# Optimization experiments

Hardware: AMD Instinct MI355X
Metric: run time of the kernel (lower is better)

Reference implementation:

```python
import jax, jax.numpy as jnp
import numpy as np

NODE_TYPES = ["drug", "protein", "side_effect", "pathway"]
N = {"drug": 20000, "protein": 50000, "side_effect": 10000, "pathway": 3000}
# (src_type, dst_type) for: treats, targets, in_pathway, causes, rev_treats, rev_targets, rev_in_pathway
RELS = [("drug", "side_effect"), ("drug", "protein"), ("protein", "pathway"),
        ("protein", "side_effect"), ("side_effect", "drug"), ("protein", "drug"),
        ("pathway", "protein")]
E = [500000, 400000, 150000, 400000, 500000, 400000, 150000]
D_IN, H, O = 128, 256, 256
EPS = 1e-5


def setup_inputs() -> dict:
    key = jax.random.key(0)
    ks = iter(jax.random.split(key, 64))
    inp = {}
    for t in NODE_TYPES:
        inp["x_" + t] = jax.random.normal(next(ks), (N[t], D_IN), jnp.float32)
    for i, (st, dt) in enumerate(RELS):
        inp[f"src_{i}"] = jax.random.randint(next(ks), (E[i],), 0, N[st], jnp.int32)
        inp[f"dst_{i}"] = jax.random.randint(next(ks), (E[i],), 0, N[dt], jnp.int32)
    sc1 = float(1.0 / np.sqrt(D_IN))
    sc2 = float(1.0 / np.sqrt(H))
    inp["W1l"] = jax.random.uniform(next(ks), (7, D_IN, H), jnp.float32, -sc1, sc1)
    inp["W1r"] = jax.random.uniform(next(ks), (7, D_IN, H), jnp.float32, -sc1, sc1)
    inp["b1"] = jax.random.uniform(next(ks), (7, H), jnp.float32, -sc1, sc1)
    inp["W2l"] = jax.random.uniform(next(ks), (7, H, O), jnp.float32, -sc2, sc2)
    inp["W2r"] = jax.random.uniform(next(ks), (7, H, O), jnp.float32, -sc2, sc2)
    inp["b2"] = jax.random.uniform(next(ks), (7, O), jnp.float32, -sc2, sc2)
    inp["g1"] = jnp.ones((H,), jnp.float32)
    inp["beta1"] = jnp.zeros((H,), jnp.float32)
    inp["g2"] = jnp.ones((O,), jnp.float32)
    inp["beta2"] = jnp.zeros((O,), jnp.float32)
    return inp


def _sage_layer(xs, srcs, dsts, Wl, Wr, b):
    # Hetero SAGEConv: per relation, mean-aggregate src features at dst,
    # project, add root transform; sum over relations per dst type.
    out = {t: None for t in NODE_TYPES}
    for i, (st, dt) in enumerate(RELS):
        msg = xs[st][srcs[i]]                                             # [E_i, d] gather
        s = jax.ops.segment_sum(msg, dsts[i], num_segments=N[dt])         # scatter-add
        cnt = jax.ops.segment_sum(jnp.ones((msg.shape[0], 1), msg.dtype),
                                  dsts[i], num_segments=N[dt])
        mean = s / jnp.maximum(cnt, 1.0)                                  # SAGE default aggr='mean'
        rel = mean @ Wl[i] + b[i] + xs[dt] @ Wr[i]                        # lin_l(agg) + lin_r(x_dst)
        out[dt] = rel if out[dt] is None else out[dt] + rel               # HeteroConv aggr='sum'
    return out


def _bn_relu(v, g, beta):
    # training-mode BatchNorm1d (biased variance) + ReLU
    mu = v.mean(0)
    var = v.var(0)
    return jax.nn.relu((v - mu) * jax.lax.rsqrt(var + EPS) * g + beta)


def reference(x_drug, x_protein, x_side_effect, x_pathway,
              W1l, W1r, b1, W2l, W2r, b2, g1, beta1, g2, beta2,
              src_0, dst_0, src_1, dst_1, src_2, dst_2, src_3, dst_3,
              src_4, dst_4, src_5, dst_5, src_6, dst_6):
    xs = {"drug": x_drug, "protein": x_protein,
          "side_effect": x_side_effect, "pathway": x_pathway}
    srcs = [src_0, src_1, src_2, src_3, src_4, src_5, src_6]
    dsts = [dst_0, dst_1, dst_2, dst_3, dst_4, dst_5, dst_6]
    h = _sage_layer(xs, srcs, dsts, W1l, W1r, b1)
    h = {t: _bn_relu(v, g1, beta1) for t, v in h.items()}
    h = _sage_layer(h, srcs, dsts, W2l, W2r, b2)
    h = {t: _bn_relu(v, g2, beta2) for t, v in h.items()}
    return (h["drug"], h["protein"], h["side_effect"], h["pathway"])
```

## Files before the change

kernel.cpp:

```cpp
#include <hip/hip_runtime.h>

#define EPS_BN 1e-5f

typedef short bf16x8 __attribute__((ext_vector_type(8)));
typedef float f32x4 __attribute__((ext_vector_type(4)));

__device__ __forceinline__ unsigned short f2b(float f)
{
    union { float f; unsigned int u; } c; c.f = f;
    unsigned int u = c.u + 0x7FFFu + ((c.u >> 16) & 1u);
    return (unsigned short)(u >> 16);
}
__device__ __forceinline__ float blo(unsigned int u)
{
    union { unsigned int u; float f; } c; c.u = u << 16; return c.f;
}
__device__ __forceinline__ float bhi(unsigned int u)
{
    union { unsigned int u; float f; } c; c.u = u & 0xFFFF0000u; return c.f;
}

__device__ __forceinline__ float dot2bf(float acc, unsigned int a, unsigned int sel)
{
    asm("v_dot2_f32_bf16 %0, %1, %2, %0" : "+v"(acc) : "v"(a), "v"(sel));
    return acc;
}

__device__ __forceinline__ void async_ld16(const unsigned short* g, unsigned short* l)
{
    __builtin_amdgcn_global_load_lds(
        (const __attribute__((address_space(1))) unsigned int*)g,
        (__attribute__((address_space(3))) unsigned int*)l, 16, 0, 0);
}

__device__ __forceinline__ int relof_e(int e) {
    return (e>=500000)+(e>=900000)+(e>=1050000)+(e>=1450000)+(e>=1950000)+(e>=2350000);
}
__device__ __forceinline__ int relof_n(int i) {
    return (i>=10000)+(i>=60000)+(i>=63000)+(i>=73000)+(i>=93000)+(i>=113000);
}
__device__ __forceinline__ int eoff_of(int r) {
    return r<1?0 : r<2?500000 : r<3?900000 : r<4?1050000 : r<5?1450000 : r<6?1950000 : 2350000;
}
__device__ __forceinline__ int coff_of(int r) {
    return r<1?0 : r<2?10000 : r<3?60000 : r<4?63000 : r<5?73000 : r<6?93000 : 113000;
}
__device__ __forceinline__ int typ_of(int row) { return (row>=20000)+(row>=70000)+(row>=80000); }
__device__ __forceinline__ float invR_of(int t){ return t<1?5e-5f : t<2?2e-5f : t<3?1e-4f : (1.0f/3000.0f); }

struct Graph { const int* src[7]; const int* dst[7]; };

__device__ __forceinline__ void relptrs(const Graph& g, int r, const int*& sp, const int*& dp)
{
    sp = g.src[0]; dp = g.dst[0];
    if (r==1){sp=g.src[1];dp=g.dst[1];}
    if (r==2){sp=g.src[2];dp=g.dst[2];}
    if (r==3){sp=g.src[3];dp=g.dst[3];}
    if (r==4){sp=g.src[4];dp=g.dst[4];}
    if (r==5){sp=g.src[5];dp=g.dst[5];}
    if (r==6){sp=g.src[6];dp=g.dst[6];}
}

__global__ void count_all(Graph g, int* __restrict__ icnt)
{
    for (int e = blockIdx.x * blockDim.x + threadIdx.x; e < 2500000; e += gridDim.x * blockDim.x) {
        int r = relof_e(e);
        const int *sp, *dp; relptrs(g, r, sp, dp);
        int le = e - eoff_of(r);
        atomicAdd(&icnt[coff_of(r) + dp[le]], 1);
    }
}

__global__ __launch_bounds__(1024)
void scan1(const int* __restrict__ icnt, int* __restrict__ scanbuf, int* __restrict__ bsums)
{
    __shared__ int lds[1024];
    int tid = threadIdx.x;
    int gid = blockIdx.x * 1024 + tid;
    int v = (gid < 163000) ? icnt[gid] : 0;
    lds[tid] = v;
    __syncthreads();
    for (int d = 1; d < 1024; d <<= 1) {
        int t = (tid >= d) ? lds[tid - d] : 0;
        __syncthreads();
        lds[tid] += t;
        __syncthreads();
    }
    scanbuf[gid] = lds[tid];
    if (tid == 1023) bsums[blockIdx.x] = lds[1023];
}

__global__ __launch_bounds__(256)
void scan2(int* __restrict__ bsums)
{
    __shared__ int lds[256];
    int tid = threadIdx.x;
    int v = (tid < 160) ? bsums[tid] : 0;
    lds[tid] = v;
    __syncthreads();
    for (int d = 1; d < 256; d <<= 1) {
        int t = (tid >= d) ? lds[tid - d] : 0;
        __syncthreads();
        lds[tid] += t;
        __syncthreads();
    }
    bsums[tid] = tid ? lds[tid - 1] : 0;
}

__global__ __launch_bounds__(256)
void scan_fix(const int* __restrict__ icnt, const int* __restrict__ scanbuf,
              const int* __restrict__ bsums, int* __restrict__ rowptrG,
              int* __restrict__ cur, float* __restrict__ inv,
              unsigned char* __restrict__ sliceid)
{
    int idx = blockIdx.x * blockDim.x + threadIdx.x;
    if (idx > 163000) return;
    int G = bsums[idx >> 10] + ((idx & 1023) ? scanbuf[idx - 1] : 0);
    rowptrG[idx] = G;
    if (idx < 163000) {
        cur[idx] = G;
        inv[idx] = 1.0f / (float)max(icnt[idx], 1);
        int s = G / 312500;
        sliceid[idx] = (unsigned char)(s > 7 ? 7 : s);
    }
}

__global__ void fill_all(Graph g, const unsigned char* __restrict__ sliceid,
                         int* __restrict__ cur, int* __restrict__ csr)
{
    const int slice = blockIdx.x & 7;
    const int bper  = gridDim.x >> 3;
    const int bidx  = blockIdx.x >> 3;
    for (int e = bidx * blockDim.x + threadIdx.x; e < 2500000; e += bper * blockDim.x) {
        int r = relof_e(e);
        const int *sp, *dp; relptrs(g, r, sp, dp);
        int le = e - eoff_of(r);
        int gidx = coff_of(r) + dp[le];
        if (sliceid[gidx] == slice)
            csr[atomicAdd(&cur[gidx], 1)] = sp[le];
    }
}

__global__ void tob16_all(const float* __restrict__ x0, const float* __restrict__ x1,
                          const float* __restrict__ x2, const float* __restrict__ x3,
                          unsigned short* __restrict__ xb)
{
    const int total = 83000 * 32;
    for (int i = blockIdx.x * blockDim.x + threadIdx.x; i < total; i += gridDim.x * blockDim.x) {
        int row = i >> 5, c4 = i & 31;
        int t = typ_of(row);
        const float* xp = (t == 0) ? x0 : (t == 1) ? x1 : (t == 2) ? x2 : x3;
        int lrow = row - (t < 1 ? 0 : t < 2 ? 20000 : t < 3 ? 70000 : 80000);
        float4 v = ((const float4*)(xp + (size_t)lrow * 128))[c4];
        uint2 o;
        o.x = (unsigned int)f2b(v.x) | ((unsigned int)f2b(v.y) << 16);
        o.y = (unsigned int)f2b(v.z) | ((unsigned int)f2b(v.w) << 16);
        ((uint2*)(xb + (size_t)row * 128))[c4] = o;
    }
}

struct GatherCfg {
    const unsigned short* X[7];
    const int* rowptrG;
    const int* csr;
    const float* inv;
    unsigned short* agg;
};

template <int D>
__global__ __launch_bounds__(256)
void gather_all(GatherCfg c)
{
    constexpr int LPE = D / 8;
    constexpr int EPW = 64 / LPE;
    constexpr int U   = 4;
    int wid = (blockIdx.x * blockDim.x + threadIdx.x) >> 6;
    if (wid >= 163000) return;
    int l = threadIdx.x & 63;
    int q = l & (LPE - 1);
    int gg = l / LPE;
    int r = relof_n(wid);
    const unsigned short* X = c.X[0];
    if (r==1) X=c.X[1];
    if (r==2) X=c.X[2];
    if (r==3) X=c.X[3];
    if (r==4) X=c.X[4];
    if (r==5) X=c.X[5];
    if (r==6) X=c.X[6];
    const unsigned short* Xq = X + q * 8;
    const int* csr = c.csr;
    int beg = c.rowptrG[wid], end = c.rowptrG[wid + 1];
    float acc[8] = {0.f,0.f,0.f,0.f,0.f,0.f,0.f,0.f};
    if (beg < end) {
        const int last = end - 1;
        for (int it = beg; it < end; it += U * EPW) {
            uint4 v[U]; unsigned int sl[U];
#pragma unroll
            for (int j = 0; j < U; ++j) {
                int idx = it + j * EPW + gg;
                int e = idx < last ? idx : last;
                int s = csr[e];
                v[j]  = *(const uint4*)(Xq + (size_t)s * D);
                sl[j] = (idx <= last) ? 0x00003F80u : 0u;
            }
#pragma unroll
            for (int j = 0; j < U; ++j) {
                unsigned int lo = sl[j], hi = sl[j] << 16;
                acc[0] = dot2bf(acc[0], v[j].x, lo);
                acc[1] = dot2bf(acc[1], v[j].x, hi);
                acc[2] = dot2bf(acc[2], v[j].y, lo);
                acc[3] = dot2bf(acc[3], v[j].y, hi);
                acc[4] = dot2bf(acc[4], v[j].z, lo);
                acc[5] = dot2bf(acc[5], v[j].z, hi);
                acc[6] = dot2bf(acc[6], v[j].w, lo);
                acc[7] = dot2bf(acc[7], v[j].w, hi);
            }
        }
    }
#pragma unroll
    for (int k = 0; k < 8; ++k) {
        if (LPE == 16) acc[k] += __shfl_xor(acc[k], 16);
        acc[k] += __shfl_xor(acc[k], 32);
    }
    if (l < LPE) {
        float inv = c.inv[wid];
        uint4 o;
        o.x = (unsigned int)f2b(acc[0]*inv) | ((unsigned int)f2b(acc[1]*inv) << 16);
        o.y = (unsigned int)f2b(acc[2]*inv) | ((unsigned int)f2b(acc[3]*inv) << 16);
        o.z = (unsigned int)f2b(acc[4]*inv) | ((unsigned int)f2b(acc[5]*inv) << 16);
        o.w = (unsigned int)f2b(acc[6]*inv) | ((unsigned int)f2b(acc[7]*inv) << 16);
        *(uint4*)(c.agg + (size_t)wid * D + q * 8) = o;
    }
}

__global__ void wtrans_kernel(const float* __restrict__ Wr, const float* __restrict__ Wl,
                              unsigned short* __restrict__ wsumT, unsigned short* __restrict__ WlT,
                              int K)
{
    const int nrel[4]  = {2, 2, 2, 1};
    const int rl[4][2] = {{4,5},{1,6},{0,3},{2,2}};
    int per = 256 * K;
    int tot = 11 * per;
    for (int idx = blockIdx.x * blockDim.x + threadIdx.x; idx < tot;
         idx += gridDim.x * blockDim.x) {
        if (idx < 4 * per) {
            int t = idx / per, rem = idx - t * per;
            int n = rem / K, k = rem - n * K;
            float s = Wr[(size_t)rl[t][0] * per + k * 256 + n];
            if (nrel[t] > 1) s += Wr[(size_t)rl[t][1] * per + k * 256 + n];
            wsumT[idx] = f2b(s);
        } else {
            int j = idx - 4 * per;
            int r = j / per, rem = j - r * per;
            int n = rem / K, k = rem - n * K;
            WlT[j] = f2b(Wl[(size_t)r * per + k * 256 + n]);
        }
    }
}

struct GemmBatch {
    const unsigned short* A0[4];
    const unsigned short* A1[4];
    const unsigned short* A2[4];
    const unsigned short* B0[4];
    const unsigned short* B1[4];
    const unsigned short* B2[4];
    float* outF;
    unsigned short* outB;
    float* stats;
    int R[4]; int bcum[4]; int rowoff[4]; int nsrc[4];
    int K, kshift, outf32;
};

__global__ __launch_bounds__(512, 4)
void gemm_mfma(GemmBatch g)
{
    __shared__ __align__(16) unsigned short Atile[2][128 * 32];
    __shared__ __align__(16) unsigned short Btile[2][256 * 32];

    const int tid = threadIdx.x;
    const int bz = blockIdx.x;
    const int t = (bz >= g.bcum[1]) + (bz >= g.bcum[2]) + (bz >= g.bcum[3]);
    const int bm = (bz - g.bcum[t]) << 7;
    const int w = tid >> 6, l = tid & 63;
    const int wr = w >> 2, wc = w & 3;

    const int R = g.R[t];
    const int K = g.K, kshift = g.kshift, kmask = K - 1;
    const unsigned short* A0t = g.A0[t];
    const unsigned short* A1t = g.A1[t];
    const unsigned short* A2t = g.A2[t];
    const unsigned short* B0t = g.B0[t];
    const unsigned short* B1t = g.B1[t];
    const unsigned short* B2t = g.B2[t];
    const int steps = (g.nsrc[t] * K) >> 5;

    const int rloc = tid >> 2;
    const int swz  = (((tid & 3) ^ ((tid >> 3) & 3)) << 3);
    const int srowA = min(bm + rloc, R - 1);
    const int wseg  = w << 9;

    auto stage = [&](int st, int buf) {
        int kglob = st << 5;
        int s  = kglob >> kshift;
        int kk = kglob & kmask;
        const unsigned short* As = (s == 0) ? A0t : (s == 1) ? A1t : A2t;
        const unsigned short* Bs = (s == 0) ? B0t : (s == 1) ? B1t : B2t;
        async_ld16(As + (size_t)srowA * K + kk + swz, &Atile[buf][wseg]);
        async_ld16(Bs + (size_t)rloc  * K + kk + swz, &Btile[buf][wseg]);
        async_ld16(Bs + (size_t)(128 + rloc) * K + kk + swz, &Btile[buf][4096 + wseg]);
    };

    f32x4 acc[4][4];
#pragma unroll
    for (int i = 0; i < 4; ++i)
#pragma unroll
        for (int j = 0; j < 4; ++j)
            acc[i][j] = (f32x4){0.f, 0.f, 0.f, 0.f};

    const int ck = l >> 4;
    const int ra = wr * 64 + (l & 15);
    const int aoff = ra * 32 + ((ck ^ ((ra >> 1) & 3)) << 3);
    const int rb = wc * 64 + (l & 15);
    const int boff = rb * 32 + ((ck ^ ((rb >> 1) & 3)) << 3);

    stage(0, 0);
    __syncthreads();
    int cur = 0;
    for (int st = 0; st < steps; ++st) {
        if (st + 1 < steps) stage(st + 1, cur ^ 1);
        const unsigned short* At = Atile[cur];
        const unsigned short* Bt = Btile[cur];
        bf16x8 af[4], bfr[4];
#pragma unroll
        for (int i = 0; i < 4; ++i) {
            af[i]  = *(const bf16x8*)(At + aoff + i * 512);
            bfr[i] = *(const bf16x8*)(Bt + boff + i * 512);
        }
#pragma unroll
        for (int mi = 0; mi < 4; ++mi)
#pragma unroll
            for (int ni = 0; ni < 4; ++ni)
                acc[mi][ni] = __builtin_amdgcn_mfma_f32_16x16x32_bf16(
                    af[mi], bfr[ni], acc[mi][ni], 0, 0, 0);
        __syncthreads();
        cur ^= 1;
    }

    const int orow0 = bm + wr * 64 + ((l >> 4) << 2);
    const int ocol0 = wc * 64 + (l & 15);
#pragma unroll
    for (int ni = 0; ni < 4; ++ni) {
        int col = ocol0 + ni * 16;
        float ps = 0.f, pq = 0.f;
#pragma unroll
        for (int mi = 0; mi < 4; ++mi) {
#pragma unroll
            for (int j = 0; j < 4; ++j) {
                int row = orow0 + mi * 16 + j;
                float v = acc[mi][ni][j];
                if (row < R) {
                    size_t o = (size_t)(g.rowoff[t] + row) * 256 + col;
                    if (g.outf32) g.outF[o] = v;
                    else          g.outB[o] = f2b(v);
                } else v = 0.f;
                ps += v; pq += v * v;
            }
        }
        ps += __shfl_xor(ps, 16); ps += __shfl_xor(ps, 32);
        pq += __shfl_xor(pq, 16); pq += __shfl_xor(pq, 32);
        if (l < 16) {
            atomicAdd(&g.stats[t * 512 + col], ps);
            atomicAdd(&g.stats[t * 512 + 256 + col], pq);
        }
    }
}

template <int F32>
__global__ __launch_bounds__(256)
void bn_apply_all(void* __restrict__ Hv, const float* __restrict__ stats,
                  const float* __restrict__ gg, const float* __restrict__ be)
{
    const int total4 = 83000 * 64;
    for (int i4 = blockIdx.x * blockDim.x + threadIdx.x; i4 < total4;
         i4 += gridDim.x * blockDim.x) {
        int row = i4 >> 6;
        int c4  = (i4 & 63) << 2;
        int t   = typ_of(row);
        float invR = invR_of(t);
        const float* st = stats + t * 512;
        float vin[4];
        if (F32) {
            float4 v = *(const float4*)((const float*)Hv + (size_t)row * 256 + c4);
            vin[0]=v.x; vin[1]=v.y; vin[2]=v.z; vin[3]=v.w;
        } else {
            uint2 u = *(const uint2*)((const unsigned short*)Hv + (size_t)row * 256 + c4);
            vin[0]=blo(u.x); vin[1]=bhi(u.x); vin[2]=blo(u.y); vin[3]=bhi(u.y);
        }
        float vout[4];
#pragma unroll
        for (int k = 0; k < 4; ++k) {
            int c = c4 + k;
            float mu  = st[c] * invR;
            float var = st[256 + c] * invR - mu * mu;
            float sc  = rsqrtf(var + EPS_BN) * gg[c];
            float v   = (vin[k] - mu) * sc + be[c];
            vout[k] = fmaxf(v, 0.f);
        }
        if (F32) {
            float4 o; o.x=vout[0]; o.y=vout[1]; o.z=vout[2]; o.w=vout[3];
            *(float4*)((float*)Hv + (size_t)row * 256 + c4) = o;
        } else {
            uint2 o;
            o.x = (unsigned int)f2b(vout[0]) | ((unsigned int)f2b(vout[1]) << 16);
            o.y = (unsigned int)f2b(vout[2]) | ((unsigned int)f2b(vout[3]) << 16);
            *(uint2*)((unsigned short*)Hv + (size_t)row * 256 + c4) = o;
        }
    }
}

extern "C" void kernel_launch(void* const* d_in, const int* in_sizes, int n_in,
                              void* d_out, int out_size, void* d_ws, size_t ws_size,
                              hipStream_t stream)
{
    static const int Nn[4]   = {20000, 50000, 10000, 3000};
    static const int roff[4] = {0, 20000, 70000, 80000};
    static const int rst[7]  = {0, 0, 1, 1, 2, 1, 3};
    static const int coff[7] = {0, 10000, 60000, 63000, 73000, 93000, 113000};
    static const int trels[4][2] = {{4,5},{1,6},{0,3},{2,2}};
    static const int tnrel[4]    = {2, 2, 2, 1};
    const int CNT_TOTAL = 163000;

    const float* x[4];
    for (int t = 0; t < 4; ++t) x[t] = (const float*)d_in[t];
    Graph graph;
    for (int i = 0; i < 7; ++i) {
        graph.src[i] = (const int*)d_in[4 + 2 * i];
        graph.dst[i] = (const int*)d_in[5 + 2 * i];
    }
    const float* W1l = (const float*)d_in[18];
    const float* W1r = (const float*)d_in[19];
    const float* W2l = (const float*)d_in[21];
    const float* W2r = (const float*)d_in[22];
    const float* g1  = (const float*)d_in[24];
    const float* be1 = (const float*)d_in[25];
    const float* g2  = (const float*)d_in[26];
    const float* be2 = (const float*)d_in[27];
    float* out = (float*)d_out;
    (void)n_in; (void)in_sizes; (void)out_size; (void)ws_size;

    char* w = (char*)d_ws;
    size_t off = 0;
    auto carve = [&](size_t bytes) -> void* {
        void* p = (void*)(w + off);
        off = (off + bytes + 255) & ~(size_t)255;
        return p;
    };
    int*   icnt    = (int*)carve((size_t)CNT_TOTAL * 4);
    int*   cur     = (int*)carve((size_t)CNT_TOTAL * 4);
    int*   rowptrG = (int*)carve((size_t)(CNT_TOTAL + 1) * 4);
    int*   csr     = (int*)carve((size_t)2500000 * 4);
    int*   scanbuf = (int*)carve((size_t)163840 * 4);
    int*   bsums   = (int*)carve((size_t)256 * 4);
    float* inv     = (float*)carve((size_t)CNT_TOTAL * 4);
    float* stats   = (float*)carve((size_t)2 * 4 * 512 * 4);
    unsigned char* sliceid = (unsigned char*)carve((size_t)CNT_TOTAL);
    unsigned short* wsumT1 = (unsigned short*)carve((size_t)4 * 256 * 128 * 2);
    unsigned short* WlT1   = (unsigned short*)carve((size_t)7 * 256 * 128 * 2);
    unsigned short* wsumT2 = (unsigned short*)carve((size_t)4 * 256 * 256 * 2);
    unsigned short* WlT2   = (unsigned short*)carve((size_t)7 * 256 * 256 * 2);
    unsigned short* U      = (unsigned short*)carve((size_t)163000 * 256 * 2);
    unsigned short* hb     = (unsigned short*)carve((size_t)83000 * 256 * 2);
    unsigned short* xb    = U;
    unsigned short* aggL1 = U + (size_t)83000 * 128;
    unsigned short* aggL2 = U;
    float* stats1 = stats;
    float* stats2 = stats + 2048;

    hipMemsetAsync(icnt, 0, (size_t)CNT_TOTAL * 4, stream);
    hipMemsetAsync(stats, 0, (size_t)2 * 4 * 512 * 4, stream);
    count_all<<<2048, 256, 0, stream>>>(graph, icnt);
    scan1<<<160, 1024, 0, stream>>>(icnt, scanbuf, bsums);
    scan2<<<1, 256, 0, stream>>>(bsums);
    scan_fix<<<(CNT_TOTAL + 256) / 256, 256, 0, stream>>>(icnt, scanbuf, bsums,
                                                          rowptrG, cur, inv, sliceid);
    fill_all<<<2048, 256, 0, stream>>>(graph, sliceid, cur, csr);

    tob16_all<<<2048, 256, 0, stream>>>(x[0], x[1], x[2], x[3], xb);
    wtrans_kernel<<<1024, 256, 0, stream>>>(W1r, W1l, wsumT1, WlT1, 128);
    wtrans_kernel<<<1024, 256, 0, stream>>>(W2r, W2l, wsumT2, WlT2, 256);

    for (int layer = 0; layer < 2; ++layer) {
        const int K = layer ? 256 : 128;
        const float* gg = layer ? g2  : g1;
        const float* be = layer ? be2 : be1;
        unsigned short* agg = layer ? aggL2 : aggL1;
        unsigned short* wsumT = layer ? wsumT2 : wsumT1;
        unsigned short* WlT   = layer ? WlT2   : WlT1;
        float* st = layer ? stats2 : stats1;

        GatherCfg gc;
        for (int r = 0; r < 7; ++r)
            gc.X[r] = layer ? (hb + (size_t)roff[rst[r]] * 256)
                            : (xb + (size_t)roff[rst[r]] * 128);
        gc.rowptrG = rowptrG; gc.csr = csr; gc.inv = inv; gc.agg = agg;
        if (layer == 0) gather_all<128><<<40750, 256, 0, stream>>>(gc);
        else            gather_all<256><<<40750, 256, 0, stream>>>(gc);

        GemmBatch gb;
        for (int t = 0; t < 4; ++t) {
            gb.A0[t] = layer ? (hb + (size_t)roff[t] * 256) : (xb + (size_t)roff[t] * 128);
            gb.A1[t] = agg + (size_t)coff[trels[t][0]] * K;
            gb.A2[t] = (tnrel[t] > 1) ? (agg + (size_t)coff[trels[t][1]] * K) : gb.A1[t];
            gb.B0[t] = wsumT + (size_t)t * 256 * K;
            gb.B1[t] = WlT + (size_t)trels[t][0] * 256 * K;
            gb.B2[t] = (tnrel[t] > 1) ? (WlT + (size_t)trels[t][1] * 256 * K) : gb.B1[t];
            gb.R[t] = Nn[t];
            gb.rowoff[t] = roff[t];
            gb.nsrc[t] = 1 + tnrel[t];
        }
        gb.bcum[0] = 0; gb.bcum[1] = 157; gb.bcum[2] = 548; gb.bcum[3] = 627;
        gb.outF = out; gb.outB = hb;
        gb.stats = st;
        gb.K = K; gb.kshift = layer ? 8 : 7; gb.outf32 = layer;
        gemm_mfma<<<651, 512, 0, stream>>>(gb);

        if (layer == 0) bn_apply_all<0><<<2048, 256, 0, stream>>>(hb, st, gg, be);
        else            bn_apply_all<1><<<2048, 256, 0, stream>>>(out, st, gg, be);
    }
}
```

Measured before the change: 778.6 us.

## Build CSR via two-pass bucketed fill with per-bucket atomics and LDS scatter

Replaces the per-destination atomic CSR fill with a two-stage scheme. Edges are first appended into 16-destination buckets using one atomic counter per bucket, packed as local-index and source pairs. A second kernel then scatters each bucket into final CSR order through shared memory. This aims to spread contention and produce more coalesced writes, at the cost of an extra pass over the edges and reuse of the hb buffer as scratch.

New measurement: 956.1 us. 22.8% more time.

```diff
diff --git a/kernel.cpp b/kernel.cpp
--- a/kernel.cpp
+++ b/kernel.cpp
@@ -1,6 +1,8 @@
 #include <hip/hip_runtime.h>
 
 #define EPS_BN 1e-5f
+#define FS_CAP 4096
+#define NBUCK 10188
 
 typedef short bf16x8 __attribute__((ext_vector_type(8)));
 typedef float f32x4 __attribute__((ext_vector_type(4)));
@@ -110,23 +112,26 @@
 __global__ __launch_bounds__(256)
 void scan_fix(const int* __restrict__ icnt, const int* __restrict__ scanbuf,
               const int* __restrict__ bsums, int* __restrict__ rowptrG,
-              int* __restrict__ cur, float* __restrict__ inv,
-              unsigned char* __restrict__ sliceid)
+              float* __restrict__ inv, int* __restrict__ bcur,
+              unsigned char* __restrict__ sliceB)
 {
     int idx = blockIdx.x * blockDim.x + threadIdx.x;
     if (idx > 163000) return;
     int G = bsums[idx >> 10] + ((idx & 1023) ? scanbuf[idx - 1] : 0);
     rowptrG[idx] = G;
     if (idx < 163000) {
-        cur[idx] = G;
         inv[idx] = 1.0f / (float)max(icnt[idx], 1);
-        int s = G / 312500;
-        sliceid[idx] = (unsigned char)(s > 7 ? 7 : s);
-    }
-}
-
-__global__ void fill_all(Graph g, const unsigned char* __restrict__ sliceid,
-                         int* __restrict__ cur, int* __restrict__ csr)
+        if ((idx & 15) == 0) {
+            int bk = idx >> 4;
+            bcur[bk] = G;
+            int s = G / 312500;
+            sliceB[bk] = (unsigned char)(s > 7 ? 7 : s);
+        }
+    }
+}
+
+__global__ void fill_pairs(Graph g, const unsigned char* __restrict__ sliceB,
+                           int* __restrict__ bcur, unsigned int* __restrict__ pairs)
 {
     const int slice = blockIdx.x & 7;
     const int bper  = gridDim.x >> 3;
@@ -136,8 +141,48 @@
         const int *sp, *dp; relptrs(g, r, sp, dp);
         int le = e - eoff_of(r);
         int gidx = coff_of(r) + dp[le];
-        if (sliceid[gidx] == slice)
-            csr[atomicAdd(&cur[gidx], 1)] = sp[le];
+        int bk = gidx >> 4;
+        if (sliceB[bk] == slice) {
+            int pos = atomicAdd(&bcur[bk], 1);
+            pairs[pos] = ((unsigned int)(gidx & 15) << 17) | (unsigned int)sp[le];
+        }
+    }
+}
+
+__global__ __launch_bounds__(256)
+void fill_scatter(const unsigned int* __restrict__ pairs, const int* __restrict__ rowptrG,
+                  int* __restrict__ csr)
+{
+    __shared__ int rp[17];
+    __shared__ int cnt[16];
+    __shared__ int buf[FS_CAP];
+    int bk = blockIdx.x;
+    int d0 = bk << 4;
+    int nd = min(16, 163000 - d0);
+    int tid = threadIdx.x;
+    if (tid <= nd) rp[tid] = rowptrG[d0 + tid];
+    if (tid < 16) cnt[tid] = 0;
+    __syncthreads();
+    int base = rp[0];
+    int total = rp[nd] - base;
+    if (total <= FS_CAP) {
+        for (int i = tid; i < total; i += 256) {
+            unsigned int p = pairs[base + i];
+            int local = p >> 17;
+            int src   = p & 0x1FFFF;
+            int ofs = rp[local] - base + atomicAdd(&cnt[local], 1);
+            buf[ofs] = src;
+        }
+        __syncthreads();
+        for (int i = tid; i < total; i += 256)
+            csr[base + i] = buf[i];
+    } else {
+        for (int i = tid; i < total; i += 256) {
+            unsigned int p = pairs[base + i];
+            int local = p >> 17;
+            int src   = p & 0x1FFFF;
+            csr[rp[local] + atomicAdd(&cnt[local], 1)] = src;
+        }
     }
 }
 
@@ -457,14 +502,14 @@
         return p;
     };
     int*   icnt    = (int*)carve((size_t)CNT_TOTAL * 4);
-    int*   cur     = (int*)carve((size_t)CNT_TOTAL * 4);
+    int*   bcur    = (int*)carve((size_t)NBUCK * 4);
     int*   rowptrG = (int*)carve((size_t)(CNT_TOTAL + 1) * 4);
     int*   csr     = (int*)carve((size_t)2500000 * 4);
     int*   scanbuf = (int*)carve((size_t)163840 * 4);
     int*   bsums   = (int*)carve((size_t)256 * 4);
     float* inv     = (float*)carve((size_t)CNT_TOTAL * 4);
     float* stats   = (float*)carve((size_t)2 * 4 * 512 * 4);
-    unsigned char* sliceid = (unsigned char*)carve((size_t)CNT_TOTAL);
+    unsigned char* sliceB = (unsigned char*)carve((size_t)NBUCK);
     unsigned short* wsumT1 = (unsigned short*)carve((size_t)4 * 256 * 128 * 2);
     unsigned short* WlT1   = (unsigned short*)carve((size_t)7 * 256 * 128 * 2);
     unsigned short* wsumT2 = (unsigned short*)carve((size_t)4 * 256 * 256 * 2);
@@ -474,6 +519,7 @@
     unsigned short* xb    = U;
     unsigned short* aggL1 = U + (size_t)83000 * 128;
     unsigned short* aggL2 = U;
+    unsigned int* pairs = (unsigned int*)hb;
     float* stats1 = stats;
     float* stats2 = stats + 2048;
 
@@ -483,8 +529,9 @@
     scan1<<<160, 1024, 0, stream>>>(icnt, scanbuf, bsums);
     scan2<<<1, 256, 0, stream>>>(bsums);
     scan_fix<<<(CNT_TOTAL + 256) / 256, 256, 0, stream>>>(icnt, scanbuf, bsums,
-                                                          rowptrG, cur, inv, sliceid);
-    fill_all<<<2048, 256, 0, stream>>>(graph, sliceid, cur, csr);
+                                                          rowptrG, inv, bcur, sliceB);
+    fill_pairs<<<2048, 256, 0, stream>>>(graph, sliceB, bcur, pairs);
+    fill_scatter<<<NBUCK, 256, 0, stream>>>(pairs, rowptrG, csr);
 
     tob16_all<<<2048, 256, 0, stream>>>(x[0], x[1], x[2], x[3], xb);
     wtrans_kernel<<<1024, 256, 0, stream>>>(W1r, W1l, wsumT1, WlT1, 128);
```
